# Performance work log

Measured on AMD Instinct MI355X. Metric: run time of the kernel, lower is better.

The kernel has to match this reference:

```python
import jax, jax.numpy as jnp
import numpy as np

B, M, IN, H, D = 64, 512, 256, 4, 64
N = B * M
E = N * 16


def setup_inputs() -> dict:
    key = jax.random.key(0)
    ks = jax.random.split(key, 12)
    s = 1.0 / np.sqrt(IN)
    return {
        "query_input": jax.random.normal(ks[0], (N, IN), jnp.float32),
        "source_input": jax.random.normal(ks[1], (N, IN), jnp.float32),
        "edge_weight": jax.random.uniform(ks[2], (E,), jnp.float32),
        "Wq_w": jax.random.normal(ks[3], (IN, H * D), jnp.float32) * s,
        "Wq_b": jax.random.normal(ks[4], (H * D,), jnp.float32) * s,
        "Wk_w": jax.random.normal(ks[5], (IN, H * D), jnp.float32) * s,
        "Wk_b": jax.random.normal(ks[6], (H * D,), jnp.float32) * s,
        "Wv_w": jax.random.normal(ks[7], (IN, H * D), jnp.float32) * s,
        "Wv_b": jax.random.normal(ks[8], (H * D,), jnp.float32) * s,
        "n_nodes": jnp.full((B,), M, jnp.int32),
        "edge_index": jax.random.randint(ks[9], (2, E), 0, N, jnp.int32),
    }


def reference(query_input, source_input, edge_weight, Wq_w, Wq_b, Wk_w, Wk_b, Wv_w, Wv_b, n_nodes, edge_index):
    # projections -> [N, H, D]
    q = (query_input @ Wq_w + Wq_b).reshape(N, H, D)
    k = (source_input @ Wk_w + Wk_b).reshape(N, H, D)
    v = (source_input @ Wv_w + Wv_b).reshape(N, H, D)

    # 'simple' kernel attention. Global L2 normalization (torch.norm over whole tensor).
    qn = q / jnp.linalg.norm(q)
    kn = k / jnp.linalg.norm(k)
    # equal-size graphs: padding + mask reduces exactly to a reshape [B, M, H, D]
    q_pad = qn.reshape(B, M, H, D)
    k_pad = kn.reshape(B, M, H, D)
    v_pad = v.reshape(B, M, H, D)
    kv = jnp.einsum('bmhk,bmhv->bhkv', k_pad, v_pad)          # per-graph K^T V
    v_sum = v_pad.sum(axis=1)                                  # [B, H, D] scatter_add over batch
    k_sum = k_pad.sum(axis=1)                                  # [B, H, D]
    numer = jnp.einsum('bmhk,bhkv->bmhv', q_pad, kv) + v_sum[:, None]
    denom = jnp.einsum('bmhk,bhk->bmh', q_pad, k_sum) + n_nodes.astype(q.dtype)[:, None, None]
    attn = (numer / denom[..., None]).reshape(N, H, D)

    # gcn_conv on value: out[c] = sum_{e: col_e = c} w_e * rsqrt(deg[col_e]*deg[row_e]) * v[row_e]
    row, col = edge_index[0], edge_index[1]
    deg = jax.ops.segment_sum(jnp.ones((E,), jnp.float32), col, num_segments=N)
    val = edge_weight / jnp.sqrt(deg[col] * deg[row])
    val = jnp.nan_to_num(val, nan=0.0, posinf=0.0, neginf=0.0)
    gcn = jax.ops.segment_sum(val[:, None, None] * v[row], col, num_segments=N)

    return (attn + gcn).mean(axis=1)  # mean over heads -> [N, D]
```

## Files before the change

### kernel.cpp

```cpp
#include <hip/hip_runtime.h>
#include <hip/hip_bf16.h>

#define NN 32768
#define BB 64
#define MM 512
#define HH 4
#define DD 64
#define INF 256
#define HD 256
#define EE 524288

typedef unsigned short ushort;
typedef unsigned int uint;
typedef short s16x8 __attribute__((ext_vector_type(8)));
typedef ushort u16x8 __attribute__((ext_vector_type(8)));
typedef float f32x4 __attribute__((ext_vector_type(4)));

__device__ __forceinline__ ushort f2bf(float f) {
    uint u = __float_as_uint(f);
    return (ushort)((u + 0x7fffu + ((u >> 16) & 1u)) >> 16);
}
__device__ __forceinline__ float bf2f(ushort u) {
    return __uint_as_float((uint)u << 16);
}
__device__ __forceinline__ uint pkbf(float x, float y) {
    __hip_bfloat162 h = __float22bfloat162_rn(make_float2(x, y));
    return *(uint*)&h;
}

__global__ __launch_bounds__(256) void prep_kernel(
    const float* __restrict__ Wq, const float* __restrict__ Wk,
    const float* __restrict__ Wv, ushort* __restrict__ WT,
    const int* __restrict__ ei, int* __restrict__ deg)
{
    const int bid = blockIdx.x;
    if (bid < 768) {
        const int id = bid * 256 + threadIdx.x;
        const int mat = id >> 16, rem = id & 65535;
        const int n = rem >> 8, kk = rem & 255;
        const float* W = (mat == 0) ? Wq : (mat == 1) ? Wk : Wv;
        WT[id] = f2bf(W[kk * 256 + n]);
    } else {
        const int e = (bid - 768) * 256 + threadIdx.x;
        atomicAdd(&deg[ei[EE + e]], 1);
    }
}

#define BKP 40
#define BPI 32
__global__ __launch_bounds__(256) void qkv_scan(
    const float* __restrict__ Xq, const float* __restrict__ Xs,
    const ushort* __restrict__ WT,
    const float* __restrict__ bq, const float* __restrict__ bk,
    const float* __restrict__ bv,
    ushort* __restrict__ qo, ushort* __restrict__ ko, ushort* __restrict__ vo,
    float* __restrict__ sumsq,
    const int* __restrict__ deg, int* __restrict__ offsets)
{
    __shared__ ushort Asu[128 * BKP];
    __shared__ ushort Bsu[128 * BPI];
    __shared__ float wred[4];
    __shared__ int part[256];

    const int id = blockIdx.x;
    const int t = threadIdx.x;

    if (id == 1536) {
        const int base = t * 128;
        int s = 0;
        for (int i = 0; i < 128; ++i) s += deg[base + i];
        part[t] = s;
        __syncthreads();
        for (int off = 1; off < 256; off <<= 1) {
            int a = part[t];
            int b2 = (t >= off) ? part[t - off] : 0;
            __syncthreads();
            part[t] = a + b2;
            __syncthreads();
        }
        int run = (t == 0) ? 0 : part[t - 1];
        for (int i = 0; i < 128; ++i) { offsets[base + i] = run; run += deg[base + i]; }
        if (t == 255) offsets[NN] = run;
        return;
    }

    const int vv = (id & 7) * 192 + (id >> 3);
    const int rt = vv / 6, ct = vv % 6;
    const int wsel = ct >> 1;
    const float* A    = (wsel == 0) ? Xq : Xs;
    const ushort* W   = WT + (size_t)wsel * 65536;
    const float* bias = (wsel == 0) ? bq : (wsel == 1) ? bk : bv;
    ushort* C         = (wsel == 0) ? qo : (wsel == 1) ? ko : vo;
    const int row0 = rt * 128;
    const int col0 = (ct & 1) * 128;

    const int l = t & 63, w = t >> 6;
    const int fr = l & 15, q4 = l >> 4;
    const int wr = (w & 1) * 64, wc = (w >> 1) * 64;
    const int sr = t >> 1, sh = (t & 1) * 16;

    f32x4 acc[4][4] = {};

    float4 a0, a1, a2, a3;
    u16x8 b0, b1;
    {
        const float* ap = &A[(size_t)(row0 + sr) * INF + sh];
        a0 = *(const float4*)(ap + 0);
        a1 = *(const float4*)(ap + 4);
        a2 = *(const float4*)(ap + 8);
        a3 = *(const float4*)(ap + 12);
        const ushort* bp = &W[(size_t)(col0 + sr) * INF + sh];
        b0 = *(const u16x8*)(bp + 0);
        b1 = *(const u16x8*)(bp + 8);
    }

    for (int it = 0; it < 8; ++it) {
        __syncthreads();
        {
            u16x8 pa0, pa1;
            pa0[0] = f2bf(a0.x); pa0[1] = f2bf(a0.y); pa0[2] = f2bf(a0.z); pa0[3] = f2bf(a0.w);
            pa0[4] = f2bf(a1.x); pa0[5] = f2bf(a1.y); pa0[6] = f2bf(a1.z); pa0[7] = f2bf(a1.w);
            pa1[0] = f2bf(a2.x); pa1[1] = f2bf(a2.y); pa1[2] = f2bf(a2.z); pa1[3] = f2bf(a2.w);
            pa1[4] = f2bf(a3.x); pa1[5] = f2bf(a3.y); pa1[6] = f2bf(a3.z); pa1[7] = f2bf(a3.w);
            *(u16x8*)&Asu[sr * BKP + sh] = pa0;
            *(u16x8*)&Asu[sr * BKP + sh + 8] = pa1;
            *(u16x8*)&Bsu[sr * BPI + sh] = b0;
            *(u16x8*)&Bsu[sr * BPI + sh + 8] = b1;
        }
        __syncthreads();

        if (it < 7) {
            const int k0 = (it + 1) * 32;
            const float* ap = &A[(size_t)(row0 + sr) * INF + k0 + sh];
            a0 = *(const float4*)(ap + 0);
            a1 = *(const float4*)(ap + 4);
            a2 = *(const float4*)(ap + 8);
            a3 = *(const float4*)(ap + 12);
            const ushort* bp = &W[(size_t)(col0 + sr) * INF + k0 + sh];
            b0 = *(const u16x8*)(bp + 0);
            b1 = *(const u16x8*)(bp + 8);
        }

        const int kg = q4 * 8;
        s16x8 af[4], bf[4];
#pragma unroll
        for (int i = 0; i < 4; ++i)
            af[i] = *(const s16x8*)&Asu[(wr + i * 16 + fr) * BKP + kg];
#pragma unroll
        for (int j = 0; j < 4; ++j)
            bf[j] = *(const s16x8*)&Bsu[(wc + j * 16 + fr) * BPI + kg];
#pragma unroll
        for (int i = 0; i < 4; ++i)
#pragma unroll
            for (int j = 0; j < 4; ++j)
                acc[i][j] = __builtin_amdgcn_mfma_f32_16x16x32_bf16(
                    af[i], bf[j], acc[i][j], 0, 0, 0);
    }

    float loc = 0.f;
#pragma unroll
    for (int j = 0; j < 4; ++j) {
        const int colg = col0 + wc + j * 16 + fr;
        const float bj = bias[colg];
#pragma unroll
        for (int i = 0; i < 4; ++i) {
            const int rowg = row0 + wr + i * 16 + q4 * 4;
#pragma unroll
            for (int m = 0; m < 4; ++m) {
                float cv = acc[i][j][m] + bj;
                loc += cv * cv;
                C[(size_t)(rowg + m) * HD + colg] = f2bf(cv);
            }
        }
    }
    if (wsel < 2) {
#pragma unroll
        for (int off = 32; off > 0; off >>= 1) loc += __shfl_down(loc, off, 64);
        if (l == 0) wred[w] = loc;
        __syncthreads();
        if (t == 0) atomicAdd(&sumsq[wsel], wred[0] + wred[1] + wred[2] + wred[3]);
    }
}

#define KVP 136
__global__ __launch_bounds__(256) void kv_vbar(
    const ushort* __restrict__ k16, const ushort* __restrict__ v16,
    float* __restrict__ kv_p, float* __restrict__ ksum_p, float* __restrict__ vsum_p,
    float* __restrict__ vbar)
{
    __shared__ ushort kT[64 * KVP];
    __shared__ ushort vT[64 * KVP];
    const int bid = blockIdx.x;
    const int t = threadIdx.x;

    if (bid >= 1024) {
        const int idx = (bid - 1024) * 1024 + t * 4;
        const int n = idx >> 6, d0 = idx & 63;
        const ushort* vr = &v16[(size_t)n * HD + d0];
        float4 o;
        float* op = (float*)&o;
#pragma unroll
        for (int j = 0; j < 4; ++j)
            op[j] = 0.25f * (bf2f(vr[j]) + bf2f(vr[64 + j]) +
                             bf2f(vr[128 + j]) + bf2f(vr[192 + j]));
        *(float4*)&vbar[idx] = o;
        return;
    }

    const int h = bid & 3, b = (bid >> 2) & 63, z = bid >> 8;
    const int l = t & 63, w = t >> 6;
    const size_t base = (size_t)b * MM * HD + (size_t)h * DD;
    const int m0 = z * 128;

    {
        const int mat = t >> 7;
        const int u = t & 63;
        const int dhalf = (t >> 6) & 1;
        const int r0 = 2 * u;
        const int d0 = dhalf * 32;
        const ushort* src = mat ? v16 : k16;
        ushort* dst = mat ? vT : kT;
        const ushort* p0 = &src[base + (size_t)(m0 + r0) * HD + d0];
        const ushort* p1 = p0 + HD;
        u16x8 ra[4], rb[4];
#pragma unroll
        for (int i = 0; i < 4; ++i) ra[i] = *(const u16x8*)(p0 + 8 * i);
#pragma unroll
        for (int i = 0; i < 4; ++i) rb[i] = *(const u16x8*)(p1 + 8 * i);
#pragma unroll
        for (int i = 0; i < 4; ++i)
#pragma unroll
            for (int jj = 0; jj < 8; ++jj) {
                const int d = d0 + 8 * i + jj;
                uint pk = (uint)ra[i][jj] | ((uint)rb[i][jj] << 16);
                *(uint*)&dst[d * KVP + r0] = pk;
            }
    }
    __syncthreads();

    const int fr = l & 15, q4 = l >> 4, kg = q4 * 8;
    const int wr2 = (w & 1) * 32, wc2 = (w >> 1) * 32;
    s16x8 ones;
#pragma unroll
    for (int i = 0; i < 8; ++i) ones[i] = (short)0x3F80;

    f32x4 acc[2][2] = {};
    f32x4 aks[2] = {};
    f32x4 avs[2] = {};
#pragma unroll
    for (int s = 0; s < 4; ++s) {
        const int mo = s * 32 + kg;
        s16x8 af[2], bf[2];
        af[0] = *(const s16x8*)&kT[(wr2 + fr) * KVP + mo];
        af[1] = *(const s16x8*)&kT[(wr2 + 16 + fr) * KVP + mo];
        bf[0] = *(const s16x8*)&vT[(wc2 + fr) * KVP + mo];
        bf[1] = *(const s16x8*)&vT[(wc2 + 16 + fr) * KVP + mo];
#pragma unroll
        for (int il = 0; il < 2; ++il)
#pragma unroll
            for (int jl = 0; jl < 2; ++jl)
                acc[il][jl] = __builtin_amdgcn_mfma_f32_16x16x32_bf16(
                    af[il], bf[jl], acc[il][jl], 0, 0, 0);
#pragma unroll
        for (int il = 0; il < 2; ++il)
            aks[il] = __builtin_amdgcn_mfma_f32_16x16x32_bf16(
                af[il], ones, aks[il], 0, 0, 0);
#pragma unroll
        for (int jl = 0; jl < 2; ++jl)
            avs[jl] = __builtin_amdgcn_mfma_f32_16x16x32_bf16(
                ones, bf[jl], avs[jl], 0, 0, 0);
    }

    float* kvb = &kv_p[(((size_t)b * HH + h) * 4 + z) * 4096];
#pragma unroll
    for (int jl = 0; jl < 2; ++jl) {
        const int dv = wc2 + 16 * jl + fr;
#pragma unroll
        for (int il = 0; il < 2; ++il) {
            const int dk = wr2 + 16 * il + q4 * 4;
            *(f32x4*)&kvb[(size_t)dv * 64 + dk] = acc[il][jl];
        }
    }
    float* ksb = &ksum_p[(((size_t)b * HH + h) * 4 + z) * 64];
    float* vsb = &vsum_p[(((size_t)b * HH + h) * 4 + z) * 64];
    if (wc2 == 0 && fr == 0) {
#pragma unroll
        for (int il = 0; il < 2; ++il)
#pragma unroll
            for (int m = 0; m < 4; ++m)
                ksb[wr2 + 16 * il + q4 * 4 + m] = aks[il][m];
    }
    if (wr2 == 0 && l < 16) {
        vsb[wc2 + l]      = avs[0][0];
        vsb[wc2 + 16 + l] = avs[1][0];
    }
}

__global__ __launch_bounds__(256) void red_bucket(
    const float* __restrict__ kv_p, const float* __restrict__ ksum_p,
    const float* __restrict__ vsum_p,
    ushort* __restrict__ kv16, float* __restrict__ ksum_f, float* __restrict__ vsum_f,
    const int* __restrict__ ei, const float* __restrict__ ew,
    const int* __restrict__ deg, const int* __restrict__ offsets,
    int* __restrict__ cursor, int2* __restrict__ pairbuf)
{
    const int bid = blockIdx.x;
    const int t = threadIdx.x;

    if (bid < 1024) {
        const int o4 = bid * 1024 + t * 4;
        const int bh = o4 >> 12, off = o4 & 4095;
        const float* p = &kv_p[(size_t)bh * 16384 + off];
        float4 s0 = *(const float4*)p;
        float4 s1 = *(const float4*)(p + 4096);
        float4 s2 = *(const float4*)(p + 8192);
        float4 s3 = *(const float4*)(p + 12288);
        const float r0 = s0.x + s1.x + s2.x + s3.x;
        const float r1 = s0.y + s1.y + s2.y + s3.y;
        const float r2 = s0.z + s1.z + s2.z + s3.z;
        const float r3 = s0.w + s1.w + s2.w + s3.w;
        uint2 pk = make_uint2(pkbf(r0, r1), pkbf(r2, r3));
        *(uint2*)&kv16[(size_t)bh * 4096 + off] = pk;
    } else if (bid < 1152) {
        const int o = (bid - 1024) * 256 + t;
        const float* src = (o < 16384) ? ksum_p : vsum_p;
        float* dst = (o < 16384) ? ksum_f : vsum_f;
        const int oo = o & 16383;
        const int bh = oo >> 6, d = oo & 63;
        const float* p = &src[(size_t)bh * 256 + d];
        dst[oo] = p[0] + p[64] + p[128] + p[192];
    } else {
        const int e = (bid - 1152) * 256 + t;
        const int row = ei[e], col = ei[EE + e];
        const long long prod = (long long)deg[row] * (long long)deg[col];
        float val = 0.f;
        if (prod > 0) val = ew[e] * __frsqrt_rn((float)prod);
        const int pos = atomicAdd(&cursor[col], 1);
        pairbuf[offsets[col] + pos] = make_int2(row, __float_as_int(val));
    }
}

#define AKP 72
__global__ __launch_bounds__(256) void attn_mfma(
    const ushort* __restrict__ q16, const ushort* __restrict__ kv16,
    const float* __restrict__ ksum_f, const float* __restrict__ vsum_f,
    const float* __restrict__ sumsq,
    const int* __restrict__ n_nodes, float* __restrict__ out)
{
    const int b = blockIdx.y;
    const int m0 = blockIdx.x * 64;
    const int t = threadIdx.x;
    const int l = t & 63, w = t >> 6;
    const int fr = l & 15, q4 = l >> 4;
    const int wn = (w & 1) * 32, wd = (w >> 1) * 32;

    __shared__ ushort kvbf[64 * AKP];
    __shared__ float ksum_l[64], vsum_l[64], denom_l[64];

    const float nn = (float)n_nodes[b];
    const float inv = 1.0f / (sqrtf(sumsq[0]) * sqrtf(sumsq[1]));
    f32x4 acco[2][2] = {};

    for (int h = 0; h < HH; ++h) {
        __syncthreads();
        {
            const int dv = t >> 2, dk0 = (t & 3) * 16;
            const ushort* kvg = &kv16[((size_t)(b * HH + h)) * 4096 + dv * 64 + dk0];
            *(uint4*)&kvbf[dv * AKP + dk0]     = *(const uint4*)kvg;
            *(uint4*)&kvbf[dv * AKP + dk0 + 8] = *(const uint4*)(kvg + 8);
        }
        if (t >= 64 && t < 128)
            ksum_l[t - 64] = ksum_f[((size_t)(b * HH + h)) * 64 + t - 64];
        else if (t >= 128 && t < 192)
            vsum_l[t - 128] = vsum_f[((size_t)(b * HH + h)) * 64 + t - 128];
        __syncthreads();

        if (t < 64) {
            const ushort* qr = &q16[((size_t)(b * MM + m0 + t)) * HD + h * DD];
            float dsum = 0.f;
#pragma unroll
            for (int c = 0; c < 8; ++c) {
                u16x8 qq = *(const u16x8*)(qr + 8 * c);
#pragma unroll
                for (int j2 = 0; j2 < 8; ++j2)
                    dsum += bf2f(qq[j2]) * ksum_l[8 * c + j2];
            }
            denom_l[t] = nn + inv * dsum;
        }
        __syncthreads();

        f32x4 pacc[2][2] = {};
#pragma unroll
        for (int kx = 0; kx < 2; ++kx) {
            const int k0 = kx * 32;
            s16x8 af[2], bf[2];
#pragma unroll
            for (int il = 0; il < 2; ++il)
                af[il] = *(const s16x8*)&q16[
                    ((size_t)(b * MM + m0 + wn + 16 * il + fr)) * HD + h * DD + k0 + q4 * 8];
#pragma unroll
            for (int jl = 0; jl < 2; ++jl)
                bf[jl] = *(const s16x8*)&kvbf[(wd + 16 * jl + fr) * AKP + k0 + q4 * 8];
#pragma unroll
            for (int il = 0; il < 2; ++il)
#pragma unroll
                for (int jl = 0; jl < 2; ++jl)
                    pacc[il][jl] = __builtin_amdgcn_mfma_f32_16x16x32_bf16(
                        af[il], bf[jl], pacc[il][jl], 0, 0, 0);
        }
#pragma unroll
        for (int il = 0; il < 2; ++il)
#pragma unroll
            for (int m = 0; m < 4; ++m) {
                const float rden = 0.25f / denom_l[wn + 16 * il + q4 * 4 + m];
#pragma unroll
                for (int jl = 0; jl < 2; ++jl) {
                    const int d = wd + 16 * jl + fr;
                    acco[il][jl][m] += (inv * pacc[il][jl][m] + vsum_l[d]) * rden;
                }
            }
    }

#pragma unroll
    for (int il = 0; il < 2; ++il)
#pragma unroll
        for (int m = 0; m < 4; ++m) {
            const size_t node = (size_t)b * MM + m0 + wn + 16 * il + q4 * 4 + m;
#pragma unroll
            for (int jl = 0; jl < 2; ++jl)
                out[node * DD + wd + 16 * jl + fr] = acco[il][jl][m];
        }
}

__global__ __launch_bounds__(256) void gcn_gather(
    const int* __restrict__ offsets, const int2* __restrict__ pairbuf,
    const float* __restrict__ vbar, float* __restrict__ out)
{
    const int t = blockIdx.x * 256 + threadIdx.x;
    const int n = t >> 6, d = t & 63;
    const int s = offsets[n], e = offsets[n + 1];
    float acc = 0.f;
    int i = s;
    for (; i + 4 <= e; i += 4) {
        const int2 p0 = pairbuf[i],     p1 = pairbuf[i + 1];
        const int2 p2 = pairbuf[i + 2], p3 = pairbuf[i + 3];
        acc += __int_as_float(p0.y) * vbar[(size_t)p0.x * DD + d];
        acc += __int_as_float(p1.y) * vbar[(size_t)p1.x * DD + d];
        acc += __int_as_float(p2.y) * vbar[(size_t)p2.x * DD + d];
        acc += __int_as_float(p3.y) * vbar[(size_t)p3.x * DD + d];
    }
    for (; i < e; ++i) {
        const int2 p = pairbuf[i];
        acc += __int_as_float(p.y) * vbar[(size_t)p.x * DD + d];
    }
    out[(size_t)n * DD + d] += acc;
}

extern "C" void kernel_launch(void* const* d_in, const int* in_sizes, int n_in,
                              void* d_out, int out_size, void* d_ws, size_t ws_size,
                              hipStream_t stream)
{
    (void)in_sizes; (void)n_in; (void)out_size; (void)ws_size;
    const float* Xq = (const float*)d_in[0];
    const float* Xs = (const float*)d_in[1];
    const float* ew = (const float*)d_in[2];
    const float* Wq = (const float*)d_in[3];
    const float* bq = (const float*)d_in[4];
    const float* Wk = (const float*)d_in[5];
    const float* bk = (const float*)d_in[6];
    const float* Wv = (const float*)d_in[7];
    const float* bv = (const float*)d_in[8];
    const int* n_nodes = (const int*)d_in[9];
    const int* ei = (const int*)d_in[10];
    float* out = (float*)d_out;
    float* ws  = (float*)d_ws;

    const size_t SZ_QKV   = (size_t)NN * HD / 2;
    const size_t OFF_Q    = 0;
    const size_t OFF_K    = SZ_QKV;
    const size_t OFF_V    = SZ_QKV * 2;
    const size_t OFF_SS   = SZ_QKV * 3;
    const size_t OFF_DEG  = OFF_SS + 16;
    const size_t OFF_CUR  = OFF_DEG + NN;
    const size_t OFF_WT   = OFF_CUR + NN;
    const size_t OFF_KV   = OFF_WT + 3 * 65536 / 2;
    const size_t OFF_KSP  = OFF_KV + (size_t)BB * HH * 4 * 4096;
    const size_t OFF_VSP  = OFF_KSP + (size_t)BB * HH * 4 * 64;
    const size_t OFF_KV16 = OFF_VSP + (size_t)BB * HH * 4 * 64;
    const size_t OFF_KSF  = OFF_KV16 + (size_t)BB * HH * 4096 / 2;
    const size_t OFF_VSF  = OFF_KSF + (size_t)BB * HH * 64;
    const size_t OFF_OFFS = OFF_VSF + (size_t)BB * HH * 64;
    const size_t OFF_PAIR = OFF_OFFS + NN + 16;
    const size_t OFF_VBAR = OFF_PAIR + 2 * (size_t)EE;

    ushort* q16   = (ushort*)(ws + OFF_Q);
    ushort* k16   = (ushort*)(ws + OFF_K);
    ushort* v16   = (ushort*)(ws + OFF_V);
    float* sumsq  = ws + OFF_SS;
    int*   deg    = (int*)(ws + OFF_DEG);
    int*   cursor = (int*)(ws + OFF_CUR);
    ushort* WT    = (ushort*)(ws + OFF_WT);
    float* kv_p   = ws + OFF_KV;
    float* ksum_p = ws + OFF_KSP;
    float* vsum_p = ws + OFF_VSP;
    ushort* kv16  = (ushort*)(ws + OFF_KV16);
    float* ksum_f = ws + OFF_KSF;
    float* vsum_f = ws + OFF_VSF;
    int*   offs   = (int*)(ws + OFF_OFFS);
    int2*  pairb  = (int2*)(ws + OFF_PAIR);
    float* vbar   = ws + OFF_VBAR;

    hipMemsetAsync(sumsq, 0, (16 + 2 * NN) * sizeof(float), stream);
    prep_kernel<<<2816, 256, 0, stream>>>(Wq, Wk, Wv, WT, ei, deg);
    qkv_scan<<<1537, 256, 0, stream>>>(
        Xq, Xs, WT, bq, bk, bv, q16, k16, v16, sumsq, deg, offs);
    kv_vbar<<<3072, 256, 0, stream>>>(k16, v16, kv_p, ksum_p, vsum_p, vbar);
    red_bucket<<<3200, 256, 0, stream>>>(
        kv_p, ksum_p, vsum_p, kv16, ksum_f, vsum_f,
        ei, ew, deg, offs, cursor, pairb);
    attn_mfma<<<dim3(MM / 64, BB), 256, 0, stream>>>(
        q16, kv16, ksum_f, vsum_f, sumsq, n_nodes, out);
    gcn_gather<<<(NN * DD) / 256, 256, 0, stream>>>(offs, pairb, vbar, out);
}
```

Before: 267.5 us.

## Use 64x64 full-K tiles for QKV GEMM and move edge bucketing earlier

The QKV projection GEMM switches from 128x128 tiles with a register-prefetched K loop to 64x64 output tiles. Each block loads the whole K=256 slice of A and B into shared memory once, then runs 8 MFMA steps with a single barrier, giving four times as many blocks. The edge bucketing work moves from the reduction kernel into the kv/vbar kernel so it runs alongside the KV partial products. The smaller tiles cut per-block data reuse, raising global and LDS traffic, and the 64-float4 register staging increases register pressure.

```diff
diff --git a/kernel.cpp b/kernel.cpp
--- a/kernel.cpp
+++ b/kernel.cpp
@@ -46,9 +46,8 @@
     }
 }
 
-#define BKP 40
-#define BPI 32
-__global__ __launch_bounds__(256) void qkv_scan(
+#define AP 264
+__global__ __launch_bounds__(256) void qkv_big(
     const float* __restrict__ Xq, const float* __restrict__ Xs,
     const ushort* __restrict__ WT,
     const float* __restrict__ bq, const float* __restrict__ bk,
@@ -57,15 +56,15 @@
     float* __restrict__ sumsq,
     const int* __restrict__ deg, int* __restrict__ offsets)
 {
-    __shared__ ushort Asu[128 * BKP];
-    __shared__ ushort Bsu[128 * BPI];
+    __shared__ ushort As[64 * AP];
+    __shared__ ushort Bs[64 * AP];
     __shared__ float wred[4];
     __shared__ int part[256];
 
     const int id = blockIdx.x;
     const int t = threadIdx.x;
 
-    if (id == 1536) {
+    if (id == 6144) {
         const int base = t * 128;
         int s = 0;
         for (int i = 0; i < 128; ++i) s += deg[base + i];
@@ -84,115 +83,102 @@
         return;
     }
 
-    const int vv = (id & 7) * 192 + (id >> 3);
-    const int rt = vv / 6, ct = vv % 6;
-    const int wsel = ct >> 1;
-    const float* A    = (wsel == 0) ? Xq : Xs;
-    const ushort* W   = WT + (size_t)wsel * 65536;
-    const float* bias = (wsel == 0) ? bq : (wsel == 1) ? bk : bv;
-    ushort* C         = (wsel == 0) ? qo : (wsel == 1) ? ko : vo;
-    const int row0 = rt * 128;
-    const int col0 = (ct & 1) * 128;
+    const int vv = (id & 7) * 768 + (id >> 3);
+    const int rt = vv / 12, rem = vv % 12;
+    const int mat = rem >> 2, ct = rem & 3;
+    const float* A    = (mat == 0) ? Xq : Xs;
+    const ushort* W   = WT + (size_t)mat * 65536;
+    const float* bias = (mat == 0) ? bq : (mat == 1) ? bk : bv;
+    ushort* C         = (mat == 0) ? qo : (mat == 1) ? ko : vo;
+    const int row0 = rt * 64;
+    const int col0 = ct * 64;
 
     const int l = t & 63, w = t >> 6;
     const int fr = l & 15, q4 = l >> 4;
-    const int wr = (w & 1) * 64, wc = (w >> 1) * 64;
-    const int sr = t >> 1, sh = (t & 1) * 16;
-
-    f32x4 acc[4][4] = {};
-
-    float4 a0, a1, a2, a3;
-    u16x8 b0, b1;
+
     {
-        const float* ap = &A[(size_t)(row0 + sr) * INF + sh];
-        a0 = *(const float4*)(ap + 0);
-        a1 = *(const float4*)(ap + 4);
-        a2 = *(const float4*)(ap + 8);
-        a3 = *(const float4*)(ap + 12);
-        const ushort* bp = &W[(size_t)(col0 + sr) * INF + sh];
-        b0 = *(const u16x8*)(bp + 0);
-        b1 = *(const u16x8*)(bp + 8);
-    }
-
-    for (int it = 0; it < 8; ++it) {
-        __syncthreads();
-        {
-            u16x8 pa0, pa1;
-            pa0[0] = f2bf(a0.x); pa0[1] = f2bf(a0.y); pa0[2] = f2bf(a0.z); pa0[3] = f2bf(a0.w);
-            pa0[4] = f2bf(a1.x); pa0[5] = f2bf(a1.y); pa0[6] = f2bf(a1.z); pa0[7] = f2bf(a1.w);
-            pa1[0] = f2bf(a2.x); pa1[1] = f2bf(a2.y); pa1[2] = f2bf(a2.z); pa1[3] = f2bf(a2.w);
-            pa1[4] = f2bf(a3.x); pa1[5] = f2bf(a3.y); pa1[6] = f2bf(a3.z); pa1[7] = f2bf(a3.w);
-            *(u16x8*)&Asu[sr * BKP + sh] = pa0;
-            *(u16x8*)&Asu[sr * BKP + sh + 8] = pa1;
-            *(u16x8*)&Bsu[sr * BPI + sh] = b0;
-            *(u16x8*)&Bsu[sr * BPI + sh + 8] = b1;
-        }
-        __syncthreads();
-
-        if (it < 7) {
-            const int k0 = (it + 1) * 32;
-            const float* ap = &A[(size_t)(row0 + sr) * INF + k0 + sh];
-            a0 = *(const float4*)(ap + 0);
-            a1 = *(const float4*)(ap + 4);
-            a2 = *(const float4*)(ap + 8);
-            a3 = *(const float4*)(ap + 12);
-            const ushort* bp = &W[(size_t)(col0 + sr) * INF + k0 + sh];
-            b0 = *(const u16x8*)(bp + 0);
-            b1 = *(const u16x8*)(bp + 8);
-        }
-
-        const int kg = q4 * 8;
-        s16x8 af[4], bf[4];
-#pragma unroll
-        for (int i = 0; i < 4; ++i)
-            af[i] = *(const s16x8*)&Asu[(wr + i * 16 + fr) * BKP + kg];
+        const int srow = t >> 2, sph = (t & 3) * 64;
+        const float* ap = &A[(size_t)(row0 + srow) * INF + sph];
+        float4 av[16];
+#pragma unroll
+        for (int i = 0; i < 16; ++i) av[i] = *(const float4*)(ap + 4 * i);
+        const ushort* bp = &W[(size_t)(col0 + srow) * INF + sph];
+        u16x8 bv8[8];
+#pragma unroll
+        for (int i = 0; i < 8; ++i) bv8[i] = *(const u16x8*)(bp + 8 * i);
+#pragma unroll
+        for (int i = 0; i < 8; ++i) {
+            uint4 pk = make_uint4(
+                pkbf(av[2 * i].x, av[2 * i].y), pkbf(av[2 * i].z, av[2 * i].w),
+                pkbf(av[2 * i + 1].x, av[2 * i + 1].y), pkbf(av[2 * i + 1].z, av[2 * i + 1].w));
+            *(uint4*)&As[srow * AP + sph + 8 * i] = pk;
+        }
+#pragma unroll
+        for (int i = 0; i < 8; ++i)
+            *(u16x8*)&Bs[srow * AP + sph + 8 * i] = bv8[i];
+    }
+    __syncthreads();
+
+    f32x4 acc[4] = {};
+#pragma unroll
+    for (int s = 0; s < 8; ++s) {
+        const int ko2 = s * 32 + q4 * 8;
+        s16x8 af = *(const s16x8*)&As[(16 * w + fr) * AP + ko2];
+        s16x8 bf[4];
 #pragma unroll
         for (int j = 0; j < 4; ++j)
-            bf[j] = *(const s16x8*)&Bsu[(wc + j * 16 + fr) * BPI + kg];
-#pragma unroll
-        for (int i = 0; i < 4; ++i)
-#pragma unroll
-            for (int j = 0; j < 4; ++j)
-                acc[i][j] = __builtin_amdgcn_mfma_f32_16x16x32_bf16(
-                    af[i], bf[j], acc[i][j], 0, 0, 0);
+            bf[j] = *(const s16x8*)&Bs[(16 * j + fr) * AP + ko2];
+#pragma unroll
+        for (int j = 0; j < 4; ++j)
+            acc[j] = __builtin_amdgcn_mfma_f32_16x16x32_bf16(af, bf[j], acc[j], 0, 0, 0);
     }
 
     float loc = 0.f;
 #pragma unroll
     for (int j = 0; j < 4; ++j) {
-        const int colg = col0 + wc + j * 16 + fr;
+        const int colg = col0 + 16 * j + fr;
         const float bj = bias[colg];
 #pragma unroll
-        for (int i = 0; i < 4; ++i) {
-            const int rowg = row0 + wr + i * 16 + q4 * 4;
-#pragma unroll
-            for (int m = 0; m < 4; ++m) {
-                float cv = acc[i][j][m] + bj;
-                loc += cv * cv;
-                C[(size_t)(rowg + m) * HD + colg] = f2bf(cv);
-            }
-        }
-    }
-    if (wsel < 2) {
+        for (int m = 0; m < 4; ++m) {
+            const int rowg = row0 + 16 * w + q4 * 4 + m;
+            float cv = acc[j][m] + bj;
+            loc += cv * cv;
+            C[(size_t)rowg * HD + colg] = f2bf(cv);
+        }
+    }
+    if (mat < 2) {
 #pragma unroll
         for (int off = 32; off > 0; off >>= 1) loc += __shfl_down(loc, off, 64);
         if (l == 0) wred[w] = loc;
         __syncthreads();
-        if (t == 0) atomicAdd(&sumsq[wsel], wred[0] + wred[1] + wred[2] + wred[3]);
+        if (t == 0) atomicAdd(&sumsq[mat], wred[0] + wred[1] + wred[2] + wred[3]);
     }
 }
 
 #define KVP 136
-__global__ __launch_bounds__(256) void kv_vbar(
+__global__ __launch_bounds__(256) void kv_vbar_bucket(
     const ushort* __restrict__ k16, const ushort* __restrict__ v16,
     float* __restrict__ kv_p, float* __restrict__ ksum_p, float* __restrict__ vsum_p,
-    float* __restrict__ vbar)
+    float* __restrict__ vbar,
+    const int* __restrict__ ei, const float* __restrict__ ew,
+    const int* __restrict__ deg, const int* __restrict__ offsets,
+    int* __restrict__ cursor, int2* __restrict__ pairbuf)
 {
     __shared__ ushort kT[64 * KVP];
     __shared__ ushort vT[64 * KVP];
     const int bid = blockIdx.x;
     const int t = threadIdx.x;
 
+    if (bid >= 3072) {
+        const int e = (bid - 3072) * 256 + t;
+        const int row = ei[e], col = ei[EE + e];
+        const long long prod = (long long)deg[row] * (long long)deg[col];
+        float val = 0.f;
+        if (prod > 0) val = ew[e] * __frsqrt_rn((float)prod);
+        const int pos = atomicAdd(&cursor[col], 1);
+        pairbuf[offsets[col] + pos] = make_int2(row, __float_as_int(val));
+        return;
+    }
     if (bid >= 1024) {
         const int idx = (bid - 1024) * 1024 + t * 4;
         const int n = idx >> 6, d0 = idx & 63;
@@ -296,13 +282,10 @@
     }
 }
 
-__global__ __launch_bounds__(256) void red_bucket(
+__global__ __launch_bounds__(256) void red_kernel(
     const float* __restrict__ kv_p, const float* __restrict__ ksum_p,
     const float* __restrict__ vsum_p,
-    ushort* __restrict__ kv16, float* __restrict__ ksum_f, float* __restrict__ vsum_f,
-    const int* __restrict__ ei, const float* __restrict__ ew,
-    const int* __restrict__ deg, const int* __restrict__ offsets,
-    int* __restrict__ cursor, int2* __restrict__ pairbuf)
+    ushort* __restrict__ kv16, float* __restrict__ ksum_f, float* __restrict__ vsum_f)
 {
     const int bid = blockIdx.x;
     const int t = threadIdx.x;
@@ -321,7 +304,7 @@
         const float r3 = s0.w + s1.w + s2.w + s3.w;
         uint2 pk = make_uint2(pkbf(r0, r1), pkbf(r2, r3));
         *(uint2*)&kv16[(size_t)bh * 4096 + off] = pk;
-    } else if (bid < 1152) {
+    } else {
         const int o = (bid - 1024) * 256 + t;
         const float* src = (o < 16384) ? ksum_p : vsum_p;
         float* dst = (o < 16384) ? ksum_f : vsum_f;
@@ -329,14 +312,6 @@
         const int bh = oo >> 6, d = oo & 63;
         const float* p = &src[(size_t)bh * 256 + d];
         dst[oo] = p[0] + p[64] + p[128] + p[192];
-    } else {
-        const int e = (bid - 1152) * 256 + t;
-        const int row = ei[e], col = ei[EE + e];
-        const long long prod = (long long)deg[row] * (long long)deg[col];
-        float val = 0.f;
-        if (prod > 0) val = ew[e] * __frsqrt_rn((float)prod);
-        const int pos = atomicAdd(&cursor[col], 1);
-        pairbuf[offsets[col] + pos] = make_int2(row, __float_as_int(val));
     }
 }
 
@@ -512,12 +487,12 @@
 
     hipMemsetAsync(sumsq, 0, (16 + 2 * NN) * sizeof(float), stream);
     prep_kernel<<<2816, 256, 0, stream>>>(Wq, Wk, Wv, WT, ei, deg);
-    qkv_scan<<<1537, 256, 0, stream>>>(
+    qkv_big<<<6145, 256, 0, stream>>>(
         Xq, Xs, WT, bq, bk, bv, q16, k16, v16, sumsq, deg, offs);
-    kv_vbar<<<3072, 256, 0, stream>>>(k16, v16, kv_p, ksum_p, vsum_p, vbar);
-    red_bucket<<<3200, 256, 0, stream>>>(
-        kv_p, ksum_p, vsum_p, kv16, ksum_f, vsum_f,
-        ei, ew, deg, offs, cursor, pairb);
+    kv_vbar_bucket<<<5120, 256, 0, stream>>>(
+        k16, v16, kv_p, ksum_p, vsum_p, vbar, ei, ew, deg, offs, cursor, pairb);
+    red_kernel<<<1152, 256, 0, stream>>>(
+        kv_p, ksum_p, vsum_p, kv16, ksum_f, vsum_f);
     attn_mfma<<<dim3(MM / 64, BB), 256, 0, stream>>>(
         q16, kv16, ksum_f, vsum_f, sumsq, n_nodes, out);
     gcn_gather<<<(NN * DD) / 256, 256, 0, stream>>>(offs, pairb, vbar, out);
```

Result: slower. 316.5 us (+18.3%).
